# Kernel tuning notes

Hardware: AMD Instinct MI355X
Metric: run time of the kernel (lower is better)

The kernel has to match this reference:

```python
import jax, jax.numpy as jnp
import numpy as np

B, N, D = 4, 256, 128
HID = 128
IN_DIM = 4 * D + 4  # h_i, h_j, |h_i-h_j|, h_i*h_j + 2 base + 2 completion feats


def setup_inputs() -> dict:
    key = jax.random.key(0)
    k1, k2, k3, k4, k5, k6, k7 = jax.random.split(key, 7)
    node_latents = jax.random.normal(k1, (B, N, D), dtype=jnp.float32)
    base_edge_logits = jax.random.normal(k2, (B, N, N), dtype=jnp.float32)
    completion_logits = jax.random.normal(k3, (B, N, N), dtype=jnp.float32)
    # MLP params (build_mlp: Linear(in,hid) -> ReLU -> Linear(hid,1) for num_layers=2)
    s1 = 1.0 / np.sqrt(IN_DIM)
    s2 = 1.0 / np.sqrt(HID)
    W1 = jax.random.uniform(k4, (IN_DIM, HID), minval=-s1, maxval=s1, dtype=jnp.float32)
    b1 = jax.random.uniform(k5, (HID,), minval=-s1, maxval=s1, dtype=jnp.float32)
    W2 = jax.random.uniform(k6, (HID, 1), minval=-s2, maxval=s2, dtype=jnp.float32)
    b2 = jax.random.uniform(k7, (1,), minval=-s2, maxval=s2, dtype=jnp.float32)
    return {"node_latents": node_latents, "base_edge_logits": base_edge_logits,
            "completion_logits": completion_logits, "W1": W1, "b1": b1, "W2": W2, "b2": b2}


def reference(node_latents, base_edge_logits, completion_logits, W1, b1, W2, b2):
    bsz, num_nodes, hidden_dim = node_latents.shape
    h_i = jnp.broadcast_to(node_latents[:, :, None, :], (bsz, num_nodes, num_nodes, hidden_dim))
    h_j = jnp.broadcast_to(node_latents[:, None, :, :], (bsz, num_nodes, num_nodes, hidden_dim))
    base = jnp.clip(base_edge_logits, -20.0, 20.0)
    comp = jnp.clip(completion_logits, -20.0, 20.0)
    pair_feat = jnp.concatenate([
        h_i, h_j, jnp.abs(h_i - h_j), h_i * h_j,
        base[..., None], jax.nn.sigmoid(base)[..., None],
        comp[..., None], jax.nn.sigmoid(comp)[..., None],
    ], axis=-1)  # [B, N, N, IN_DIM]
    hdn = jax.nn.relu(jnp.einsum('bijf,fh->bijh', pair_feat, W1) + b1)
    logits = (jnp.einsum('bijh,ho->bijo', hdn, W2) + b2)[..., 0]  # [B, N, N]
    logits = 0.5 * (logits + jnp.swapaxes(logits, 1, 2))
    diag = jnp.eye(num_nodes, dtype=bool)[None]
    return jnp.where(diag, jnp.float32(-1e9), logits)
```

## Files before the change

kernel.cpp:

```cpp
#include <hip/hip_runtime.h>
#include <cstdint>


typedef float f32x4 __attribute__((ext_vector_type(4)));

#define INV256 0.00390625f

__device__ __forceinline__ uint32_t pk4(float a, float b, float c, float d) {
  uint32_t u = __builtin_amdgcn_cvt_pk_fp8_f32(a, b, 0, false);
  u = __builtin_amdgcn_cvt_pk_fp8_f32(c, d, u, true);
  return u;
}
__device__ __forceinline__ uint32_t pkbf2(float lo, float hi) {
  uint32_t l = __builtin_bit_cast(uint32_t, lo);
  uint32_t h = __builtin_bit_cast(uint32_t, hi);
  return (l >> 16) | (h & 0xffff0000u);
}
__device__ __forceinline__ float ulo(uint32_t u) {
  return __builtin_bit_cast(float, u << 16);
}
__device__ __forceinline__ float uhi(uint32_t u) {
  return __builtin_bit_cast(float, u & 0xffff0000u);
}
__device__ __forceinline__ long mk64(uint32_t lo, uint32_t hi) {
  return (long)((((unsigned long long)hi) << 32) | lo);
}

__global__ __launch_bounds__(128) void pre_k(const float* __restrict__ node,
                                             const float* __restrict__ W1,
                                             const float* __restrict__ b1,
                                             float* __restrict__ PiB,
                                             float* __restrict__ Pjf,
                                             uint32_t* __restrict__ W1f8) {
  int bid = blockIdx.x;
  int tid = threadIdx.x;
  if (bid < 32) {
    int ks = bid >> 2, nip = (bid >> 1) & 1, wn = bid & 1;
    int lane = tid & 63, nilow = tid >> 6;
    int quad = lane >> 4, col = lane & 15;
    int h = wn * 64 + (nip * 2 + nilow) * 16 + col;
    int k0 = ks * 32 + quad * 8;
    float w[8];
#pragma unroll
    for (int t = 0; t < 8; ++t) w[t] = W1[(256 + k0 + t) * 128 + h] * 256.0f;
    uint2 u;
    u.x = pk4(w[0], w[1], w[2], w[3]);
    u.y = pk4(w[4], w[5], w[6], w[7]);
    reinterpret_cast<uint2*>(W1f8)[(bid * 64 + lane) * 2 + nilow] = u;
  } else {
    __shared__ float sN[128];
    int row = bid - 32;
    int h = tid;
    sN[h] = node[row * 128 + h];
    __syncthreads();
    float ai = 0.f, aj = 0.f;
#pragma unroll 8
    for (int d = 0; d < 128; ++d) {
      float v = sN[d];
      ai = fmaf(v, W1[d * 128 + h], ai);
      aj = fmaf(v, W1[(128 + d) * 128 + h], aj);
    }
    PiB[row * 128 + h] = 256.0f * (ai + b1[h]);
    Pjf[row * 128 + h] = 256.0f * aj;
  }
}

__global__ __launch_bounds__(256, 5) void main_k(
    const float* __restrict__ node, const float* __restrict__ baseL,
    const float* __restrict__ compL, const float* __restrict__ W1,
    const float* __restrict__ W2, const float* __restrict__ b2,
    const uint32_t* __restrict__ W1f8, const float* __restrict__ PiB,
    const float* __restrict__ Pjf, float* __restrict__ out) {
  __shared__ __align__(16) char smem[16384 + 8448 + 1024];
  char* sF = smem;
  uint32_t* sPP = reinterpret_cast<uint32_t*>(smem + 16384);
  uint4* sScal = reinterpret_cast<uint4*>(smem + 16384 + 8448);
  float* sP = reinterpret_cast<float*>(smem);

  const int tid = threadIdx.x;
  const int bx = blockIdx.x;
  const int b = bx / 528;
  const int t = bx - b * 528;
  int tI = (int)((65.0f - sqrtf(4225.0f - 8.0f * (float)t)) * 0.5f);
  tI = (tI < 0) ? 0 : (tI > 31 ? 31 : tI);
  while (((65 * tI - tI * tI) >> 1) > t) --tI;
  while (tI < 31 && ((65 * (tI + 1) - (tI + 1) * (tI + 1)) >> 1) <= t) ++tI;
  const int tJ = tI + (t - ((65 * tI - tI * tI) >> 1));
  const int I0 = tI * 8, J0 = tJ * 8;
  const int rowB = b * 256;

  const int lane = tid & 63;
  const int wn2 = tid >> 6;
  const int col = lane & 15, quad = lane >> 4;

  const int uB = ((wn2 & 1) << 1) | (wn2 >> 1);
  uint4 gB[8];
#pragma unroll
  for (int ks = 0; ks < 8; ++ks)
    gB[ks] = reinterpret_cast<const uint4*>(W1f8)[(ks * 4 + uB) * 64 + lane];

#pragma unroll
  for (int it = 0; it < 2; ++it) {
    int fidx = it * 256 + tid;
    int row = fidx >> 5, d4 = fidx & 31;
    int gr = rowB + ((row < 8) ? (I0 + row) : (J0 + row - 8));
    float4 a = reinterpret_cast<const float4*>(PiB + (size_t)gr * 128)[d4];
    float4 c = reinterpret_cast<const float4*>(Pjf + (size_t)gr * 128)[d4];
    uint4 u;
    u.x = pkbf2(a.x, c.x);
    u.y = pkbf2(a.y, c.y);
    u.z = pkbf2(a.z, c.z);
    u.w = pkbf2(a.w, c.w);
    *reinterpret_cast<uint4*>(&sPP[row * 132 + d4 * 4]) = u;
  }

  if (tid < 128) {
    int p = tid & 63, dir = tid >> 6;
    int iN = I0 + (p >> 3), jN = J0 + (p & 7);
    int rr = dir ? jN : iN, cc = dir ? iN : jN;
    float bl = fminf(fmaxf(baseL[(size_t)(rowB + rr) * 256 + cc], -20.f), 20.f);
    float cl = fminf(fmaxf(compL[(size_t)(rowB + rr) * 256 + cc], -20.f), 20.f);
    uint2 u;
    u.x = pkbf2(256.f * bl, 256.f / (1.f + __expf(-bl)));
    u.y = pkbf2(256.f * cl, 256.f / (1.f + __expf(-cl)));
    *reinterpret_cast<uint2*>(reinterpret_cast<char*>(&sScal[p]) + dir * 8) = u;
  }

  float cB0[2], cB1[2], cB2[2], cB3[2], cW2[2];
#pragma unroll
  for (int ni = 0; ni < 2; ++ni) {
    int h = (wn2 * 2 + ni) * 16 + col;
    cB0[ni] = W1[512 * 128 + h];
    cB1[ni] = W1[513 * 128 + h];
    cB2[ni] = W1[514 * 128 + h];
    cB3[ni] = W1[515 * 128 + h];
    cW2[ni] = W2[h] * INV256;
  }
  const float b2v = b2[0];

  {
    const int d4 = tid & 31;
    const int rr = tid >> 5;
    const int ks1 = d4 >> 3, qd = (d4 >> 1) & 3, kb = (d4 & 1) * 4;
    const int scolbase = 2 * qd + 4 * ks1;
    const float4 hj = *reinterpret_cast<const float4*>(node + (size_t)(rowB + J0 + rr) * 128 + d4 * 4);
#pragma unroll
    for (int ii = 0; ii < 8; ++ii) {
      const float4 hi = *reinterpret_cast<const float4*>(node + (size_t)(rowB + I0 + ii) * 128 + d4 * 4);
      uint32_t du = pk4(fabsf(hi.x - hj.x), fabsf(hi.y - hj.y),
                        fabsf(hi.z - hj.z), fabsf(hi.w - hj.w));
      uint32_t pu = pk4(hi.x * hj.x, hi.y * hj.y, hi.z * hj.z, hi.w * hj.w);
      int p = ii * 8 + rr;
      int colp = p & 15, mi = p >> 4;
      int scol = (colp + scolbase) & 15;
      uint32_t addr = mi * 512 + qd * 128 + scol * 8 + kb;
      *reinterpret_cast<uint32_t*>(sF + ks1 * 2048 + addr) = du;
      *reinterpret_cast<uint32_t*>(sF + (ks1 + 4) * 2048 + addr) = pu;
    }
  }
  __syncthreads();

  f32x4 acc[4][2] = {};
#pragma unroll
  for (int ks = 0; ks < 8; ++ks) {
    long bb0 = mk64(gB[ks].x, gB[ks].y);
    long bb1 = mk64(gB[ks].z, gB[ks].w);
    const int ascol = (col + 2 * quad + 4 * (ks & 3)) & 15;
    const char* aks = sF + ks * 2048 + quad * 128 + ascol * 8;
#pragma unroll
    for (int mi = 0; mi < 4; ++mi) {
      uint2 av = *reinterpret_cast<const uint2*>(aks + mi * 512);
      long aa = mk64(av.x, av.y);
      acc[mi][0] = __builtin_amdgcn_mfma_f32_16x16x32_fp8_fp8(aa, bb0, acc[mi][0], 0, 0, 0);
      acc[mi][1] = __builtin_amdgcn_mfma_f32_16x16x32_fp8_fp8(aa, bb1, acc[mi][1], 0, 0, 0);
    }
  }
  __syncthreads();

  uint32_t uJ[4][2];
#pragma unroll
  for (int r = 0; r < 4; ++r)
#pragma unroll
    for (int ni = 0; ni < 2; ++ni)
      uJ[r][ni] = sPP[(8 + (quad & 1) * 4 + r) * 132 + (wn2 * 2 + ni) * 16 + col];

#pragma unroll
  for (int mi = 0; mi < 4; ++mi) {
    const int ii = mi * 2 + (quad >> 1);
    uint32_t uI[2];
#pragma unroll
    for (int ni = 0; ni < 2; ++ni)
      uI[ni] = sPP[ii * 132 + (wn2 * 2 + ni) * 16 + col];
#pragma unroll
    for (int r = 0; r < 4; ++r) {
      int p = mi * 16 + quad * 4 + r;
      uint4 sc = sScal[p];
      float f0 = ulo(sc.x), f1 = uhi(sc.x), f2 = ulo(sc.y), f3 = uhi(sc.y);
      float m0 = ulo(sc.z), m1 = uhi(sc.z), m2 = ulo(sc.w), m3 = uhi(sc.w);
      float vf = 0.f, vm = 0.f;
#pragma unroll
      for (int ni = 0; ni < 2; ++ni) {
        float piI = ulo(uI[ni]), pjI = uhi(uI[ni]);
        float piJ = ulo(uJ[r][ni]), pjJ = uhi(uJ[r][ni]);
        float a = acc[mi][ni][r];
        float pf = (a + piI) + pjJ;
        pf = fmaf(f0, cB0[ni], pf);
        pf = fmaf(f1, cB1[ni], pf);
        pf = fmaf(f2, cB2[ni], pf);
        pf = fmaf(f3, cB3[ni], pf);
        float pm = (a + piJ) + pjI;
        pm = fmaf(m0, cB0[ni], pm);
        pm = fmaf(m1, cB1[ni], pm);
        pm = fmaf(m2, cB2[ni], pm);
        pm = fmaf(m3, cB3[ni], pm);
        vf = fmaf(fmaxf(pf, 0.f), cW2[ni], vf);
        vm = fmaf(fmaxf(pm, 0.f), cW2[ni], vm);
      }
      vf += __shfl_xor(vf, 1);
      vf += __shfl_xor(vf, 2);
      vm += __shfl_xor(vm, 1);
      vm += __shfl_xor(vm, 2);
      if ((col & 3) == 0) {
        int part = wn2 * 4 + (col >> 2);
        sP[p * 40 + part] = vf;
        sP[p * 40 + 20 + part] = vm;
      }
    }
  }
  __syncthreads();

  if (tid < 64) {
    int p = tid;
    const float4* pf4 = reinterpret_cast<const float4*>(sP + p * 40);
    const float4* pm4 = reinterpret_cast<const float4*>(sP + p * 40 + 20);
    float4 fa = pf4[0], fb = pf4[1], fc = pf4[2], fd = pf4[3];
    float4 ma = pm4[0], mb = pm4[1], mc = pm4[2], md = pm4[3];
    float sumF = (fa.x + fa.y + fa.z + fa.w) + (fb.x + fb.y + fb.z + fb.w) +
                 (fc.x + fc.y + fc.z + fc.w) + (fd.x + fd.y + fd.z + fd.w);
    float sumM = (ma.x + ma.y + ma.z + ma.w) + (mb.x + mb.y + mb.z + mb.w) +
                 (mc.x + mc.y + mc.z + mc.w) + (md.x + md.y + md.z + md.w);
    float val = 0.5f * (sumF + sumM) + b2v;
    int iN = I0 + (p >> 3), jN = J0 + (p & 7);
    if (iN == jN) val = -1e9f;
    out[(size_t)(rowB + iN) * 256 + jN] = val;
    out[(size_t)(rowB + jN) * 256 + iN] = val;
  }
}

extern "C" void kernel_launch(void* const* d_in, const int* in_sizes, int n_in,
                              void* d_out, int out_size, void* d_ws, size_t ws_size,
                              hipStream_t stream) {
  const float* node = (const float*)d_in[0];
  const float* baseL = (const float*)d_in[1];
  const float* compL = (const float*)d_in[2];
  const float* W1 = (const float*)d_in[3];
  const float* b1 = (const float*)d_in[4];
  const float* W2 = (const float*)d_in[5];
  const float* b2 = (const float*)d_in[6];
  float* out = (float*)d_out;

  char* ws = (char*)d_ws;
  float* PiB = (float*)(ws);
  float* Pjf = (float*)(ws + (512 << 10));
  uint32_t* W1f8 = (uint32_t*)(ws + (1024 << 10));

  pre_k<<<1056, 128, 0, stream>>>(node, W1, b1, PiB, Pjf, W1f8);
  main_k<<<2112, 256, 0, stream>>>(node, baseL, compL, W1, W2, b2, W1f8, PiB, Pjf, out);
}
```

Before: 94.53 us.

## Batch node projections per block, use DPP quad reductions, store scalars as fp32

The node-projection kernel now handles four rows per 256-thread block, splitting the Pi and Pj projections across thread halves. Each W1 load is reused across four rows, and the launch count drops from 1056 to 288 blocks. In the main kernel, shuffle-based quad reductions are replaced by DPP row permutes. Edge scalars are kept in fp32 in separate shared arrays instead of bf16-packed, and the partial-sum stride is padded to 42 to reduce bank conflicts. This raises shared memory use and changes precision slightly for the scalar features.

```diff
diff --git a/kernel.cpp b/kernel.cpp
--- a/kernel.cpp
+++ b/kernel.cpp
@@ -25,8 +25,15 @@
 __device__ __forceinline__ long mk64(uint32_t lo, uint32_t hi) {
   return (long)((((unsigned long long)hi) << 32) | lo);
 }
-
-__global__ __launch_bounds__(128) void pre_k(const float* __restrict__ node,
+__device__ __forceinline__ float qsum4(float v) {
+  v += __builtin_bit_cast(float, __builtin_amdgcn_update_dpp(
+           0, __builtin_bit_cast(int, v), 0xB1, 0xF, 0xF, true));
+  v += __builtin_bit_cast(float, __builtin_amdgcn_update_dpp(
+           0, __builtin_bit_cast(int, v), 0x4E, 0xF, 0xF, true));
+  return v;
+}
+
+__global__ __launch_bounds__(256) void pre_k(const float* __restrict__ node,
                                              const float* __restrict__ W1,
                                              const float* __restrict__ b1,
                                              float* __restrict__ PiB,
@@ -35,34 +42,51 @@
   int bid = blockIdx.x;
   int tid = threadIdx.x;
   if (bid < 32) {
-    int ks = bid >> 2, nip = (bid >> 1) & 1, wn = bid & 1;
-    int lane = tid & 63, nilow = tid >> 6;
-    int quad = lane >> 4, col = lane & 15;
-    int h = wn * 64 + (nip * 2 + nilow) * 16 + col;
-    int k0 = ks * 32 + quad * 8;
-    float w[8];
-#pragma unroll
-    for (int t = 0; t < 8; ++t) w[t] = W1[(256 + k0 + t) * 128 + h] * 256.0f;
-    uint2 u;
-    u.x = pk4(w[0], w[1], w[2], w[3]);
-    u.y = pk4(w[4], w[5], w[6], w[7]);
-    reinterpret_cast<uint2*>(W1f8)[(bid * 64 + lane) * 2 + nilow] = u;
-  } else {
-    __shared__ float sN[128];
-    int row = bid - 32;
-    int h = tid;
-    sN[h] = node[row * 128 + h];
-    __syncthreads();
-    float ai = 0.f, aj = 0.f;
-#pragma unroll 8
-    for (int d = 0; d < 128; ++d) {
-      float v = sN[d];
-      ai = fmaf(v, W1[d * 128 + h], ai);
-      aj = fmaf(v, W1[(128 + d) * 128 + h], aj);
-    }
-    PiB[row * 128 + h] = 256.0f * (ai + b1[h]);
-    Pjf[row * 128 + h] = 256.0f * aj;
-  }
+    if (tid < 128) {
+      int ks = bid >> 2, nip = (bid >> 1) & 1, wn = bid & 1;
+      int lane = tid & 63, nilow = tid >> 6;
+      int quad = lane >> 4, col = lane & 15;
+      int h = wn * 64 + (nip * 2 + nilow) * 16 + col;
+      int k0 = ks * 32 + quad * 8;
+      float w[8];
+#pragma unroll
+      for (int t = 0; t < 8; ++t) w[t] = W1[(256 + k0 + t) * 128 + h] * 256.0f;
+      uint2 u;
+      u.x = pk4(w[0], w[1], w[2], w[3]);
+      u.y = pk4(w[4], w[5], w[6], w[7]);
+      reinterpret_cast<uint2*>(W1f8)[(bid * 64 + lane) * 2 + nilow] = u;
+    }
+    return;
+  }
+  __shared__ float sN[512];
+  const int r0 = (bid - 32) * 4;
+  {
+    int d = tid & 127, rh = tid >> 7;
+#pragma unroll
+    for (int rr = 0; rr < 2; ++rr) {
+      int row = rr * 2 + rh;
+      sN[d * 4 + row] = node[(size_t)(r0 + row) * 128 + d];
+    }
+  }
+  __syncthreads();
+  const int h = tid & 127, proj = tid >> 7;
+  const float* Wp = W1 + (size_t)proj * 128 * 128 + h;
+  float a0 = 0.f, a1 = 0.f, a2 = 0.f, a3 = 0.f;
+#pragma unroll 4
+  for (int d = 0; d < 128; ++d) {
+    float w = Wp[(size_t)d * 128];
+    float4 v = *reinterpret_cast<const float4*>(&sN[d * 4]);
+    a0 = fmaf(v.x, w, a0);
+    a1 = fmaf(v.y, w, a1);
+    a2 = fmaf(v.z, w, a2);
+    a3 = fmaf(v.w, w, a3);
+  }
+  float bb = (proj == 0) ? b1[h] : 0.f;
+  float* dst = (proj == 0) ? PiB : Pjf;
+  dst[(size_t)(r0 + 0) * 128 + h] = 256.f * (a0 + bb);
+  dst[(size_t)(r0 + 1) * 128 + h] = 256.f * (a1 + bb);
+  dst[(size_t)(r0 + 2) * 128 + h] = 256.f * (a2 + bb);
+  dst[(size_t)(r0 + 3) * 128 + h] = 256.f * (a3 + bb);
 }
 
 __global__ __launch_bounds__(256, 5) void main_k(
@@ -71,10 +95,10 @@
     const float* __restrict__ W2, const float* __restrict__ b2,
     const uint32_t* __restrict__ W1f8, const float* __restrict__ PiB,
     const float* __restrict__ Pjf, float* __restrict__ out) {
-  __shared__ __align__(16) char smem[16384 + 8448 + 1024];
+  __shared__ __align__(16) char smem[16384];
+  __shared__ __align__(16) uint32_t sPP[16 * 132];
+  __shared__ __align__(16) float sScal[64 * 12];
   char* sF = smem;
-  uint32_t* sPP = reinterpret_cast<uint32_t*>(smem + 16384);
-  uint4* sScal = reinterpret_cast<uint4*>(smem + 16384 + 8448);
   float* sP = reinterpret_cast<float*>(smem);
 
   const int tid = threadIdx.x;
@@ -120,10 +144,12 @@
     int rr = dir ? jN : iN, cc = dir ? iN : jN;
     float bl = fminf(fmaxf(baseL[(size_t)(rowB + rr) * 256 + cc], -20.f), 20.f);
     float cl = fminf(fmaxf(compL[(size_t)(rowB + rr) * 256 + cc], -20.f), 20.f);
-    uint2 u;
-    u.x = pkbf2(256.f * bl, 256.f / (1.f + __expf(-bl)));
-    u.y = pkbf2(256.f * cl, 256.f / (1.f + __expf(-cl)));
-    *reinterpret_cast<uint2*>(reinterpret_cast<char*>(&sScal[p]) + dir * 8) = u;
+    float4 v;
+    v.x = 256.f * bl;
+    v.y = 256.f / (1.f + __expf(-bl));
+    v.z = 256.f * cl;
+    v.w = 256.f / (1.f + __expf(-cl));
+    *reinterpret_cast<float4*>(&sScal[p * 12 + dir * 4]) = v;
   }
 
   float cB0[2], cB1[2], cB2[2], cB3[2], cW2[2];
@@ -194,9 +220,8 @@
 #pragma unroll
     for (int r = 0; r < 4; ++r) {
       int p = mi * 16 + quad * 4 + r;
-      uint4 sc = sScal[p];
-      float f0 = ulo(sc.x), f1 = uhi(sc.x), f2 = ulo(sc.y), f3 = uhi(sc.y);
-      float m0 = ulo(sc.z), m1 = uhi(sc.z), m2 = ulo(sc.w), m3 = uhi(sc.w);
+      float4 scf = *reinterpret_cast<const float4*>(&sScal[p * 12]);
+      float4 scm = *reinterpret_cast<const float4*>(&sScal[p * 12 + 4]);
       float vf = 0.f, vm = 0.f;
 #pragma unroll
       for (int ni = 0; ni < 2; ++ni) {
@@ -204,26 +229,24 @@
         float piJ = ulo(uJ[r][ni]), pjJ = uhi(uJ[r][ni]);
         float a = acc[mi][ni][r];
         float pf = (a + piI) + pjJ;
-        pf = fmaf(f0, cB0[ni], pf);
-        pf = fmaf(f1, cB1[ni], pf);
-        pf = fmaf(f2, cB2[ni], pf);
-        pf = fmaf(f3, cB3[ni], pf);
+        pf = fmaf(scf.x, cB0[ni], pf);
+        pf = fmaf(scf.y, cB1[ni], pf);
+        pf = fmaf(scf.z, cB2[ni], pf);
+        pf = fmaf(scf.w, cB3[ni], pf);
         float pm = (a + piJ) + pjI;
-        pm = fmaf(m0, cB0[ni], pm);
-        pm = fmaf(m1, cB1[ni], pm);
-        pm = fmaf(m2, cB2[ni], pm);
-        pm = fmaf(m3, cB3[ni], pm);
+        pm = fmaf(scm.x, cB0[ni], pm);
+        pm = fmaf(scm.y, cB1[ni], pm);
+        pm = fmaf(scm.z, cB2[ni], pm);
+        pm = fmaf(scm.w, cB3[ni], pm);
         vf = fmaf(fmaxf(pf, 0.f), cW2[ni], vf);
         vm = fmaf(fmaxf(pm, 0.f), cW2[ni], vm);
       }
-      vf += __shfl_xor(vf, 1);
-      vf += __shfl_xor(vf, 2);
-      vm += __shfl_xor(vm, 1);
-      vm += __shfl_xor(vm, 2);
+      vf = qsum4(vf);
+      vm = qsum4(vm);
       if ((col & 3) == 0) {
         int part = wn2 * 4 + (col >> 2);
-        sP[p * 40 + part] = vf;
-        sP[p * 40 + 20 + part] = vm;
+        sP[p * 42 + part] = vf;
+        sP[p * 42 + 20 + part] = vm;
       }
     }
   }
@@ -231,14 +254,15 @@
 
   if (tid < 64) {
     int p = tid;
-    const float4* pf4 = reinterpret_cast<const float4*>(sP + p * 40);
-    const float4* pm4 = reinterpret_cast<const float4*>(sP + p * 40 + 20);
-    float4 fa = pf4[0], fb = pf4[1], fc = pf4[2], fd = pf4[3];
-    float4 ma = pm4[0], mb = pm4[1], mc = pm4[2], md = pm4[3];
-    float sumF = (fa.x + fa.y + fa.z + fa.w) + (fb.x + fb.y + fb.z + fb.w) +
-                 (fc.x + fc.y + fc.z + fc.w) + (fd.x + fd.y + fd.z + fd.w);
-    float sumM = (ma.x + ma.y + ma.z + ma.w) + (mb.x + mb.y + mb.z + mb.w) +
-                 (mc.x + mc.y + mc.z + mc.w) + (md.x + md.y + md.z + md.w);
+    const float2* f2 = reinterpret_cast<const float2*>(sP + p * 42);
+    const float2* m2 = reinterpret_cast<const float2*>(sP + p * 42 + 20);
+    float sumF = 0.f, sumM = 0.f;
+#pragma unroll
+    for (int c = 0; c < 8; ++c) {
+      float2 a = f2[c], d = m2[c];
+      sumF += a.x + a.y;
+      sumM += d.x + d.y;
+    }
     float val = 0.5f * (sumF + sumM) + b2v;
     int iN = I0 + (p >> 3), jN = J0 + (p & 7);
     if (iN == jN) val = -1e9f;
@@ -264,6 +288,6 @@
   float* Pjf = (float*)(ws + (512 << 10));
   uint32_t* W1f8 = (uint32_t*)(ws + (1024 << 10));
 
-  pre_k<<<1056, 128, 0, stream>>>(node, W1, b1, PiB, Pjf, W1f8);
+  pre_k<<<288, 256, 0, stream>>>(node, W1, b1, PiB, Pjf, W1f8);
   main_k<<<2112, 256, 0, stream>>>(node, baseL, compL, W1, W2, b2, W1f8, PiB, Pjf, out);
 }
```

After: 95.75 us. Within noise of the previous version (+1.3%).
